# Kernel optimization log

Measured on AMD Instinct MI355X. Metric: run time of the kernel, lower is better.

## Reference

```python
import jax, jax.numpy as jnp
import numpy as np

N = 50000        # nodes
E = 1_600_000    # edges
F_IN = 128
HID = 128
OUT = 128
NEG_SLOPE = 0.2  # PyG GATConv default


def _gat_layer(x, src, dst, W, a_src, a_dst, b, n_nodes):
    """PyG GATConv (heads=1, add_self_loops handled by caller)."""
    h = x @ W                                   # [N, d_out]
    alpha_src = h @ a_src                       # [N]
    alpha_dst = h @ a_dst                       # [N]
    e = jax.nn.leaky_relu(alpha_src[src] + alpha_dst[dst], NEG_SLOPE)  # [E']
    # segment softmax over incoming edges of each destination node
    m = jax.ops.segment_max(e, dst, num_segments=n_nodes)
    e = jnp.exp(e - m[dst])
    s = jax.ops.segment_sum(e, dst, num_segments=n_nodes)
    alpha = e / s[dst]                          # [E']
    out = jax.ops.segment_sum(alpha[:, None] * h[src], dst, num_segments=n_nodes)
    return out + b


def setup_inputs() -> dict:
    key = jax.random.key(0)
    ks = jax.random.split(key, 11)
    sW1 = 1.0 / np.sqrt(F_IN)
    sW2 = 1.0 / np.sqrt(HID)
    return {
        "x": jax.random.normal(ks[0], (N, F_IN), dtype=jnp.float32),
        "edge_index": jax.random.randint(ks[1], (2, E), 0, N, dtype=jnp.int64
                                         if jax.config.jax_enable_x64 else jnp.int32),
        "W1": jax.random.normal(ks[2], (F_IN, HID), dtype=jnp.float32) * sW1,
        "a1_src": jax.random.normal(ks[3], (HID,), dtype=jnp.float32) * sW2,
        "a1_dst": jax.random.normal(ks[4], (HID,), dtype=jnp.float32) * sW2,
        "b1": jnp.zeros((HID,), dtype=jnp.float32),
        "W2": jax.random.normal(ks[5], (HID, OUT), dtype=jnp.float32) * sW2,
        "a2_src": jax.random.normal(ks[6], (OUT,), dtype=jnp.float32) * sW2,
        "a2_dst": jax.random.normal(ks[7], (OUT,), dtype=jnp.float32) * sW2,
        "b2": jnp.zeros((OUT,), dtype=jnp.float32),
    }


def reference(x, edge_index, W1, a1_src, a1_dst, b1, W2, a2_src, a2_dst, b2):
    n = x.shape[0]
    loop = jnp.arange(n, dtype=edge_index.dtype)
    src = jnp.concatenate([edge_index[0], loop])   # add self loops (PyG default)
    dst = jnp.concatenate([edge_index[1], loop])
    h = _gat_layer(x, src, dst, W1, a1_src, a1_dst, b1, n)
    h = jax.nn.relu(h)
    # F.dropout with training=False is identity (eval-mode reference)
    out = _gat_layer(h, src, dst, W2, a2_src, a2_dst, b2, n)
    return out
```

## Files before the change

### kernel.cpp

```cpp
#include <hip/hip_runtime.h>
#include <hip/hip_bf16.h>
#include <hip/hip_fp16.h>

#define FD 128
#define CBW 64
#define NB_MAX 1024

typedef _Float16 half8 __attribute__((ext_vector_type(8)));
typedef float f32x4 __attribute__((ext_vector_type(4)));

__global__ __launch_bounds__(256) void k_chist(const int* __restrict__ dst,
                                               int* __restrict__ ccnt, int e, int nb) {
    __shared__ int lh[NB_MAX];
    for (int i = threadIdx.x; i < nb; i += 256) lh[i] = 0;
    __syncthreads();
    for (int i = blockIdx.x * 256 + threadIdx.x; i < e; i += gridDim.x * 256)
        atomicAdd(&lh[dst[i] >> 6], 1);
    __syncthreads();
    for (int i = threadIdx.x; i < nb; i += 256) {
        int c = lh[i];
        if (c) atomicAdd(&ccnt[i], c);
    }
}

__global__ void k_cscan(const int* __restrict__ ccnt, int* __restrict__ cbase,
                        int* __restrict__ ccur, int nb, int* __restrict__ rowptr, int n) {
    __shared__ int wsum[16];
    __shared__ int woff[17];
    const int t = threadIdx.x, lane = t & 63, wid = t >> 6;
    int carry = 0;
    for (int base = 0; base < nb; base += 1024) {
        int idx = base + t;
        int v = (idx < nb) ? ccnt[idx] : 0;
        int s = v;
#pragma unroll
        for (int off = 1; off < 64; off <<= 1) {
            int u = __shfl_up(s, off, 64);
            if (lane >= off) s += u;
        }
        if (lane == 63) wsum[wid] = s;
        __syncthreads();
        if (wid == 0) {
            int w2 = (lane < 16) ? wsum[lane] : 0;
#pragma unroll
            for (int off = 1; off < 16; off <<= 1) {
                int u = __shfl_up(w2, off, 64);
                if (lane >= off) w2 += u;
            }
            if (lane < 16) woff[lane + 1] = w2;
            if (lane == 0) woff[0] = 0;
        }
        __syncthreads();
        int excl = carry + woff[wid] + (s - v);
        if (idx < nb) { cbase[idx] = excl; ccur[idx] = excl; }
        carry += woff[16];
        __syncthreads();
    }
    if (t == 0) { cbase[nb] = carry; rowptr[n] = carry; }
}

__global__ __launch_bounds__(256) void k_cscatter(const int* __restrict__ src,
                                                  const int* __restrict__ dst,
                                                  int* __restrict__ ccur,
                                                  int* __restrict__ ebuf,
                                                  int e, int nb, int nblocks) {
    __shared__ int lh[NB_MAX];
    __shared__ int lb[NB_MAX];
    const int per = (e + nblocks - 1) / nblocks;
    const int lo = blockIdx.x * per;
    const int hi = min(e, lo + per);
    const int t = threadIdx.x;
    for (int i = t; i < nb; i += 256) lh[i] = 0;
    __syncthreads();
    for (int i = lo + t; i < hi; i += 256) atomicAdd(&lh[dst[i] >> 6], 1);
    __syncthreads();
    for (int i = t; i < nb; i += 256) {
        int c = lh[i];
        lb[i] = c ? atomicAdd(&ccur[i], c) : 0;
    }
    __syncthreads();
    for (int i = t; i < nb; i += 256) lh[i] = 0;
    __syncthreads();
    for (int i = lo + t; i < hi; i += 256) {
        int d = dst[i];
        int bkt = d >> 6;
        int r = atomicAdd(&lh[bkt], 1);
        ebuf[lb[bkt] + r] = (src[i] << 6) | (d & (CBW - 1));
    }
}

__global__ __launch_bounds__(256) void k_fine(const int* __restrict__ ebuf,
                                              const int* __restrict__ cbase,
                                              int* __restrict__ rowptr,
                                              int* __restrict__ colidx, int n) {
    const int b = blockIdx.x;
    const int node0 = b * CBW;
    const int nloc = min(CBW, n - node0);
    const int beg = cbase[b], end = cbase[b + 1];
    __shared__ int fh[CBW];
    __shared__ int fo[CBW];
    const int t = threadIdx.x;
    if (t < CBW) fh[t] = 0;
    __syncthreads();
    for (int e = beg + t; e < end; e += 256) atomicAdd(&fh[ebuf[e] & (CBW - 1)], 1);
    __syncthreads();
    if (t < 64) {
        int v = fh[t];
        int s = v;
#pragma unroll
        for (int off = 1; off < 64; off <<= 1) {
            int u = __shfl_up(s, off, 64);
            if (t >= off) s += u;
        }
        fo[t] = s - v;
    }
    __syncthreads();
    if (t < nloc) rowptr[node0 + t] = beg + fo[t];
    if (t < CBW) fh[t] = 0;
    __syncthreads();
    for (int e = beg + t; e < end; e += 256) {
        int v = ebuf[e];
        int d = v & (CBW - 1);
        int r = atomicAdd(&fh[d], 1);
        colidx[beg + fo[d] + r] = v >> 6;
    }
}

__global__ __launch_bounds__(1024) void k_prep(const float* __restrict__ W1,
                                               const float* __restrict__ W2,
                                               __half* __restrict__ T1,
                                               __half* __restrict__ T2,
                                               const float* __restrict__ x,
                                               __half* __restrict__ x16, int count8) {
    const int t = threadIdx.x;
    if (blockIdx.x < 2) {
        __shared__ float sw[128 * 129];
        const float* W = blockIdx.x ? W2 : W1;
        __half* T = blockIdx.x ? T2 : T1;
#pragma unroll
        for (int i = 0; i < 16; i++) {
            int idx = i * 1024 + t;
            sw[(idx >> 7) * 129 + (idx & 127)] = W[idx];
        }
        __syncthreads();
#pragma unroll
        for (int i = 0; i < 8; i++) {
            int o = i * 1024 + t;
            int c = o >> 6, kp = o & 63;
            float lo = sw[(kp * 2) * 129 + c];
            float hi = sw[(kp * 2 + 1) * 129 + c];
            *(__half2*)&T[c * 128 + kp * 2] = __floats2half2_rn(lo, hi);
        }
    } else {
        int i = (blockIdx.x - 2) * 1024 + t;
        if (i >= count8) return;
        float4 a = *(const float4*)&x[(size_t)i * 8];
        float4 b = *(const float4*)&x[(size_t)i * 8 + 4];
        union { __half2 h2[4]; uint4 u; } pk;
        pk.h2[0] = __floats2half2_rn(a.x, a.y);
        pk.h2[1] = __floats2half2_rn(a.z, a.w);
        pk.h2[2] = __floats2half2_rn(b.x, b.y);
        pk.h2[3] = __floats2half2_rn(b.z, b.w);
        *(uint4*)&x16[(size_t)i * 8] = pk.u;
    }
}

__global__ __launch_bounds__(256) void k_gemm(const __half* __restrict__ X,
                                              const __half* __restrict__ Wt,
                                              const float* __restrict__ a_s,
                                              const float* __restrict__ a_d,
                                              __half* __restrict__ H,
                                              float* __restrict__ as_,
                                              float* __restrict__ ad_, int n) {
    const int t = threadIdx.x;
    const int wave = t >> 6, lane = t & 63;
    const int g = lane >> 4, c16 = lane & 15;
    const int row0 = blockIdx.x * 64 + wave * 16;

    half8 A[4];
    {
        int row = row0 + c16;
        int rc = (row < n) ? row : (n - 1);
        const __half* xp = &X[(size_t)rc * 128 + g * 8];
#pragma unroll
        for (int kc = 0; kc < 4; kc++) A[kc] = *(const half8*)(xp + kc * 32);
    }

    f32x4 acc[8];
#pragma unroll
    for (int ct = 0; ct < 8; ct++) acc[ct] = (f32x4){0.f, 0.f, 0.f, 0.f};

#pragma unroll
    for (int ct = 0; ct < 8; ct++) {
        const __half* wp = &Wt[(ct * 16 + c16) * 128 + g * 8];
#pragma unroll
        for (int kc = 0; kc < 4; kc++) {
            half8 b = *(const half8*)(wp + kc * 32);
            acc[ct] = __builtin_amdgcn_mfma_f32_16x16x32_f16(A[kc], b, acc[ct], 0, 0, 0);
        }
    }

    float asv[8], adv[8];
#pragma unroll
    for (int ct = 0; ct < 8; ct++) {
        asv[ct] = a_s[ct * 16 + c16];
        adv[ct] = a_d[ct * 16 + c16];
    }
#pragma unroll
    for (int r = 0; r < 4; r++) {
        const int row = row0 + g * 4 + r;
        float vs = 0.f, vd = 0.f;
#pragma unroll
        for (int ct = 0; ct < 8; ct++) {
            float v = acc[ct][r];
            vs += v * asv[ct];
            vd += v * adv[ct];
            if (row < n) H[(size_t)row * 128 + ct * 16 + c16] = __float2half(v);
        }
#pragma unroll
        for (int off = 8; off; off >>= 1) {
            vs += __shfl_xor(vs, off, 16);
            vd += __shfl_xor(vd, off, 16);
        }
        if (c16 == 0 && row < n) { as_[row] = vs; ad_[row] = vd; }
    }
}

__device__ __forceinline__ void fmix8(float* acc, uint4 hv, float w) {
    union { uint4 u; _Float16 h[8]; } c;
    c.u = hv;
#pragma unroll
    for (int j = 0; j < 8; j++) acc[j] += w * (float)c.h[j];
}

__global__ __launch_bounds__(256) void k_aggr(const __half* __restrict__ H,
                                              const float* __restrict__ as_,
                                              const float* __restrict__ ad_,
                                              const int* __restrict__ rowptr,
                                              const int* __restrict__ colidx,
                                              const float* __restrict__ bias,
                                              float* __restrict__ outf,
                                              __half* __restrict__ outh,
                                              int n, int mode) {
    const int wid = threadIdx.x >> 6;
    const int lane = threadIdx.x & 63;
    const int node = blockIdx.x * 4 + wid;
    if (node >= n) return;
    const int q = lane >> 4;
    const int boff = (lane & 15) * 16;
    const float adn = ad_[node];
    float sp = 0.f;
    float acc[8] = {0.f, 0.f, 0.f, 0.f, 0.f, 0.f, 0.f, 0.f};
    const int beg = rowptr[node], end = rowptr[node + 1];

    {
        float e = as_[node] + adn;
        e = (e > 0.f) ? e : 0.2f * e;
        const float w = __expf(e);
        if (lane == 63) sp += w;
        if (q == 3) {
            const uint4 hv = *(const uint4*)((const char*)H + (((unsigned)node << 8) + boff));
            fmix8(acc, hv, w);
        }
    }

    for (int it = beg; it < end; it += 64) {
        const int idx = it + lane;
        const bool valid = idx < end;
        const int idxc = valid ? idx : (end - 1);
        const int sl = colidx[idxc];
        float e = as_[sl] + adn;
        e = (e > 0.f) ? e : 0.2f * e;
        const float w = valid ? __expf(e) : 0.f;
        sp += w;
        int m = end - it; if (m > 64) m = 64;
        const int iters = (m + 3) >> 2;
        int slot = q;
#pragma unroll 4
        for (int g = 0; g < iters; ++g) {
            const int srcg = __shfl(sl, slot, 64);
            const float wg = __shfl(w, slot, 64);
            const uint4 hv = *(const uint4*)((const char*)H + (((unsigned)srcg << 8) + boff));
            fmix8(acc, hv, wg);
            slot += 4;
        }
    }

#pragma unroll
    for (int off = 1; off < 64; off <<= 1) sp += __shfl_xor(sp, off);
#pragma unroll
    for (int off = 16; off <= 32; off <<= 1) {
#pragma unroll
        for (int j = 0; j < 8; j++) acc[j] += __shfl_xor(acc[j], off);
    }
    if (q == 0) {
        const int f0 = boff >> 1;
        const float inv = 1.f / sp;
        float o[8];
        const float4 b0 = *(const float4*)&bias[f0];
        const float4 b1 = *(const float4*)&bias[f0 + 4];
        o[0] = acc[0] * inv + b0.x; o[1] = acc[1] * inv + b0.y;
        o[2] = acc[2] * inv + b0.z; o[3] = acc[3] * inv + b0.w;
        o[4] = acc[4] * inv + b1.x; o[5] = acc[5] * inv + b1.y;
        o[6] = acc[6] * inv + b1.z; o[7] = acc[7] * inv + b1.w;
        if (mode == 1) {
#pragma unroll
            for (int j = 0; j < 8; j++) o[j] = fmaxf(o[j], 0.f);
            union { __half2 h2[4]; uint4 u; } pk;
            pk.h2[0] = __floats2half2_rn(o[0], o[1]);
            pk.h2[1] = __floats2half2_rn(o[2], o[3]);
            pk.h2[2] = __floats2half2_rn(o[4], o[5]);
            pk.h2[3] = __floats2half2_rn(o[6], o[7]);
            *(uint4*)&outh[(size_t)node * 128 + f0] = pk.u;
        } else {
            *(float4*)&outf[(size_t)node * 128 + f0] = make_float4(o[0], o[1], o[2], o[3]);
            *(float4*)&outf[(size_t)node * 128 + f0 + 4] = make_float4(o[4], o[5], o[6], o[7]);
        }
    }
}

extern "C" void kernel_launch(void* const* d_in, const int* in_sizes, int n_in,
                              void* d_out, int out_size, void* d_ws, size_t ws_size,
                              hipStream_t stream) {
    const float* x   = (const float*)d_in[0];
    const int*   ei  = (const int*)d_in[1];
    const float* W1  = (const float*)d_in[2];
    const float* a1s = (const float*)d_in[3];
    const float* a1d = (const float*)d_in[4];
    const float* b1  = (const float*)d_in[5];
    const float* W2  = (const float*)d_in[6];
    const float* a2s = (const float*)d_in[7];
    const float* a2d = (const float*)d_in[8];
    const float* b2  = (const float*)d_in[9];
    float* dout = (float*)d_out;

    const int n = in_sizes[0] / FD;
    const int E = in_sizes[1] / 2;
    const int* src = ei;
    const int* dst = ei + E;
    const int NB = (n + CBW - 1) / CBW;

    char* base = (char*)d_ws;
    __half* buf0  = (__half*)base;
    int*    ebuf  = (int*)base;
    __half* H     = (__half*)(base + (size_t)n * FD * sizeof(__half));
    float* as_    = (float*)((char*)H + (size_t)n * FD * sizeof(__half));
    float* ad_    = as_ + n;
    int*   rowptr = (int*)(ad_ + n);
    int*   ccnt   = rowptr + (n + 1);
    int*   cbase  = ccnt + NB;
    int*   ccur   = cbase + NB + 1;
    int*   colidx = ccur + NB;
    size_t wt_off = (((size_t)((char*)(colidx + E) - base)) + 15) & ~(size_t)15;
    __half* Wt1h  = (__half*)(base + wt_off);
    __half* Wt2h  = Wt1h + 128 * 128;

    hipMemsetAsync(ccnt, 0, (size_t)NB * sizeof(int), stream);
    k_chist<<<256, 256, 0, stream>>>(dst, ccnt, E, NB);
    k_cscan<<<1, 1024, 0, stream>>>(ccnt, cbase, ccur, NB, rowptr, n);
    const int SCAT_BLOCKS = 256;
    k_cscatter<<<SCAT_BLOCKS, 256, 0, stream>>>(src, dst, ccur, ebuf, E, NB, SCAT_BLOCKS);
    k_fine<<<NB, 256, 0, stream>>>(ebuf, cbase, rowptr, colidx, n);

    const int count8 = n * FD / 8;
    const int prep_grid = 2 + (count8 + 1023) / 1024;
    k_prep<<<prep_grid, 1024, 0, stream>>>(W1, W2, Wt1h, Wt2h, x, buf0, count8);

    const int gemm_grid = (n + 63) / 64;
    const int node_grid = (n + 3) / 4;

    k_gemm<<<gemm_grid, 256, 0, stream>>>(buf0, Wt1h, a1s, a1d, H, as_, ad_, n);
    k_aggr<<<node_grid, 256, 0, stream>>>(H, as_, ad_, rowptr, colidx, b1,
                                          nullptr, buf0, n, 1);

    k_gemm<<<gemm_grid, 256, 0, stream>>>(buf0, Wt2h, a2s, a2d, H, as_, ad_, n);
    k_aggr<<<node_grid, 256, 0, stream>>>(H, as_, ad_, rowptr, colidx, b2,
                                          dout, nullptr, n, 0);
}
```

Before: 237.9 us.

## Fuse CSR build stages with weight transpose and layer-1 GEMM, pack aggregation shuffles

Merges the destination histogram with the weight transpose/convert, and the edge scatter with the first-layer GEMM, in shared grids. The GEMM now reads fp32 x directly, so the separate x-to-fp16 conversion pass goes away. Bucket width grows from 64 to 256 nodes, which turns the coarse scan into a single pass and makes the fine sort work across full 256-thread blocks. In aggregation, the source index and the fp16-rounded edge weight are packed into one int, so only one shuffle is needed per gathered edge. The packing assumes node ids fit in 16 bits and adds fp16 rounding of the unnormalized attention weights, with a possible overflow risk.

```diff
diff --git a/kernel.cpp b/kernel.cpp
--- a/kernel.cpp
+++ b/kernel.cpp
@@ -3,23 +3,48 @@
 #include <hip/hip_fp16.h>
 
 #define FD 128
-#define CBW 64
-#define NB_MAX 1024
+#define CBW 256
+#define NBK 256
 
 typedef _Float16 half8 __attribute__((ext_vector_type(8)));
 typedef float f32x4 __attribute__((ext_vector_type(4)));
 
-__global__ __launch_bounds__(256) void k_chist(const int* __restrict__ dst,
-                                               int* __restrict__ ccnt, int e, int nb) {
-    __shared__ int lh[NB_MAX];
-    for (int i = threadIdx.x; i < nb; i += 256) lh[i] = 0;
-    __syncthreads();
-    for (int i = blockIdx.x * 256 + threadIdx.x; i < e; i += gridDim.x * 256)
-        atomicAdd(&lh[dst[i] >> 6], 1);
-    __syncthreads();
-    for (int i = threadIdx.x; i < nb; i += 256) {
-        int c = lh[i];
-        if (c) atomicAdd(&ccnt[i], c);
+__global__ __launch_bounds__(256) void k_pre(const int* __restrict__ dst,
+                                             int* __restrict__ ccnt, int e, int nb,
+                                             const float* __restrict__ W1,
+                                             const float* __restrict__ W2,
+                                             __half* __restrict__ T1,
+                                             __half* __restrict__ T2) {
+    __shared__ float sw[128 * 129];
+    const int t = threadIdx.x;
+    if (blockIdx.x < 256) {
+        int* lh = (int*)sw;
+        if (t < NBK) lh[t] = 0;
+        __syncthreads();
+        for (int i = blockIdx.x * 256 + t; i < e; i += 256 * 256)
+            atomicAdd(&lh[dst[i] >> 8], 1);
+        __syncthreads();
+        if (t < nb) {
+            int c = lh[t];
+            if (c) atomicAdd(&ccnt[t], c);
+        }
+    } else {
+        const float* W = (blockIdx.x == 257) ? W2 : W1;
+        __half* T = (blockIdx.x == 257) ? T2 : T1;
+#pragma unroll
+        for (int i = 0; i < 64; i++) {
+            int idx = i * 256 + t;
+            sw[(idx >> 7) * 129 + (idx & 127)] = W[idx];
+        }
+        __syncthreads();
+#pragma unroll
+        for (int i = 0; i < 32; i++) {
+            int o = i * 256 + t;
+            int c = o >> 6, kp = o & 63;
+            float lo = sw[(kp * 2) * 129 + c];
+            float hi = sw[(kp * 2 + 1) * 129 + c];
+            *(__half2*)&T[c * 128 + kp * 2] = __floats2half2_rn(lo, hi);
+        }
     }
 }
 
@@ -28,64 +53,126 @@
     __shared__ int wsum[16];
     __shared__ int woff[17];
     const int t = threadIdx.x, lane = t & 63, wid = t >> 6;
-    int carry = 0;
-    for (int base = 0; base < nb; base += 1024) {
-        int idx = base + t;
-        int v = (idx < nb) ? ccnt[idx] : 0;
-        int s = v;
-#pragma unroll
-        for (int off = 1; off < 64; off <<= 1) {
-            int u = __shfl_up(s, off, 64);
-            if (lane >= off) s += u;
-        }
-        if (lane == 63) wsum[wid] = s;
-        __syncthreads();
-        if (wid == 0) {
-            int w2 = (lane < 16) ? wsum[lane] : 0;
-#pragma unroll
-            for (int off = 1; off < 16; off <<= 1) {
-                int u = __shfl_up(w2, off, 64);
-                if (lane >= off) w2 += u;
+    int v = (t < nb) ? ccnt[t] : 0;
+    int s = v;
+#pragma unroll
+    for (int off = 1; off < 64; off <<= 1) {
+        int u = __shfl_up(s, off, 64);
+        if (lane >= off) s += u;
+    }
+    if (lane == 63) wsum[wid] = s;
+    __syncthreads();
+    if (wid == 0) {
+        int w2 = (lane < 16) ? wsum[lane] : 0;
+#pragma unroll
+        for (int off = 1; off < 16; off <<= 1) {
+            int u = __shfl_up(w2, off, 64);
+            if (lane >= off) w2 += u;
+        }
+        if (lane < 16) woff[lane + 1] = w2;
+        if (lane == 0) woff[0] = 0;
+    }
+    __syncthreads();
+    int excl = woff[wid] + (s - v);
+    if (t < nb) { cbase[t] = excl; ccur[t] = excl; }
+    if (t == 0) { cbase[nb] = woff[16]; rowptr[n] = woff[16]; }
+}
+
+__global__ __launch_bounds__(256) void k_mid(const int* __restrict__ src,
+                                             const int* __restrict__ dst,
+                                             int* __restrict__ ccur,
+                                             int* __restrict__ ebuf,
+                                             int e, int nb, int nscat,
+                                             const float* __restrict__ X,
+                                             const __half* __restrict__ Wt,
+                                             const float* __restrict__ a_s,
+                                             const float* __restrict__ a_d,
+                                             __half* __restrict__ H,
+                                             float* __restrict__ as_,
+                                             float* __restrict__ ad_, int n) {
+    __shared__ int lh[NBK];
+    __shared__ int lb[NBK];
+    const int t = threadIdx.x;
+    if ((int)blockIdx.x < nscat) {
+        const int per = (e + nscat - 1) / nscat;
+        const int lo = blockIdx.x * per;
+        const int hi = min(e, lo + per);
+        if (t < NBK) lh[t] = 0;
+        __syncthreads();
+        for (int i = lo + t; i < hi; i += 256) atomicAdd(&lh[dst[i] >> 8], 1);
+        __syncthreads();
+        if (t < nb) {
+            int c = lh[t];
+            lb[t] = c ? atomicAdd(&ccur[t], c) : 0;
+        }
+        __syncthreads();
+        if (t < NBK) lh[t] = 0;
+        __syncthreads();
+        for (int i = lo + t; i < hi; i += 256) {
+            int d = dst[i];
+            int bkt = d >> 8;
+            int r = atomicAdd(&lh[bkt], 1);
+            ebuf[lb[bkt] + r] = (src[i] << 8) | (d & (CBW - 1));
+        }
+    } else {
+        const int bid = blockIdx.x - nscat;
+        const int wave = t >> 6, lane = t & 63;
+        const int g = lane >> 4, c16 = lane & 15;
+        const int row0 = bid * 64 + wave * 16;
+
+        half8 A[4];
+        {
+            int row = row0 + c16;
+            int rc = (row < n) ? row : (n - 1);
+            const float* xp = &X[(size_t)rc * 128 + g * 8];
+#pragma unroll
+            for (int kc = 0; kc < 4; kc++) {
+                float4 x0 = *(const float4*)(xp + kc * 32);
+                float4 x1 = *(const float4*)(xp + kc * 32 + 4);
+                half8 a;
+                a[0] = (_Float16)x0.x; a[1] = (_Float16)x0.y;
+                a[2] = (_Float16)x0.z; a[3] = (_Float16)x0.w;
+                a[4] = (_Float16)x1.x; a[5] = (_Float16)x1.y;
+                a[6] = (_Float16)x1.z; a[7] = (_Float16)x1.w;
+                A[kc] = a;
             }
-            if (lane < 16) woff[lane + 1] = w2;
-            if (lane == 0) woff[0] = 0;
-        }
-        __syncthreads();
-        int excl = carry + woff[wid] + (s - v);
-        if (idx < nb) { cbase[idx] = excl; ccur[idx] = excl; }
-        carry += woff[16];
-        __syncthreads();
-    }
-    if (t == 0) { cbase[nb] = carry; rowptr[n] = carry; }
-}
-
-__global__ __launch_bounds__(256) void k_cscatter(const int* __restrict__ src,
-                                                  const int* __restrict__ dst,
-                                                  int* __restrict__ ccur,
-                                                  int* __restrict__ ebuf,
-                                                  int e, int nb, int nblocks) {
-    __shared__ int lh[NB_MAX];
-    __shared__ int lb[NB_MAX];
-    const int per = (e + nblocks - 1) / nblocks;
-    const int lo = blockIdx.x * per;
-    const int hi = min(e, lo + per);
-    const int t = threadIdx.x;
-    for (int i = t; i < nb; i += 256) lh[i] = 0;
-    __syncthreads();
-    for (int i = lo + t; i < hi; i += 256) atomicAdd(&lh[dst[i] >> 6], 1);
-    __syncthreads();
-    for (int i = t; i < nb; i += 256) {
-        int c = lh[i];
-        lb[i] = c ? atomicAdd(&ccur[i], c) : 0;
-    }
-    __syncthreads();
-    for (int i = t; i < nb; i += 256) lh[i] = 0;
-    __syncthreads();
-    for (int i = lo + t; i < hi; i += 256) {
-        int d = dst[i];
-        int bkt = d >> 6;
-        int r = atomicAdd(&lh[bkt], 1);
-        ebuf[lb[bkt] + r] = (src[i] << 6) | (d & (CBW - 1));
+        }
+        f32x4 acc[8];
+#pragma unroll
+        for (int ct = 0; ct < 8; ct++) acc[ct] = (f32x4){0.f, 0.f, 0.f, 0.f};
+#pragma unroll
+        for (int ct = 0; ct < 8; ct++) {
+            const __half* wp = &Wt[(ct * 16 + c16) * 128 + g * 8];
+#pragma unroll
+            for (int kc = 0; kc < 4; kc++) {
+                half8 b = *(const half8*)(wp + kc * 32);
+                acc[ct] = __builtin_amdgcn_mfma_f32_16x16x32_f16(A[kc], b, acc[ct], 0, 0, 0);
+            }
+        }
+        float asv[8], adv[8];
+#pragma unroll
+        for (int ct = 0; ct < 8; ct++) {
+            asv[ct] = a_s[ct * 16 + c16];
+            adv[ct] = a_d[ct * 16 + c16];
+        }
+#pragma unroll
+        for (int r = 0; r < 4; r++) {
+            const int row = row0 + g * 4 + r;
+            float vs = 0.f, vd = 0.f;
+#pragma unroll
+            for (int ct = 0; ct < 8; ct++) {
+                float v = acc[ct][r];
+                vs += v * asv[ct];
+                vd += v * adv[ct];
+                if (row < n) H[(size_t)row * 128 + ct * 16 + c16] = __float2half(v);
+            }
+#pragma unroll
+            for (int off = 8; off; off >>= 1) {
+                vs += __shfl_xor(vs, off, 16);
+                vd += __shfl_xor(vd, off, 16);
+            }
+            if (c16 == 0 && row < n) { as_[row] = vs; ad_[row] = vd; }
+        }
     }
 }
 
@@ -99,69 +186,36 @@
     const int beg = cbase[b], end = cbase[b + 1];
     __shared__ int fh[CBW];
     __shared__ int fo[CBW];
-    const int t = threadIdx.x;
-    if (t < CBW) fh[t] = 0;
+    __shared__ int wt4[4];
+    const int t = threadIdx.x, lane = t & 63, wid = t >> 6;
+    fh[t] = 0;
     __syncthreads();
     for (int e = beg + t; e < end; e += 256) atomicAdd(&fh[ebuf[e] & (CBW - 1)], 1);
     __syncthreads();
-    if (t < 64) {
+    {
         int v = fh[t];
         int s = v;
 #pragma unroll
         for (int off = 1; off < 64; off <<= 1) {
             int u = __shfl_up(s, off, 64);
-            if (t >= off) s += u;
-        }
-        fo[t] = s - v;
+            if (lane >= off) s += u;
+        }
+        if (lane == 63) wt4[wid] = s;
+        __syncthreads();
+        int wo = 0;
+#pragma unroll
+        for (int j = 0; j < 4; j++) wo += (j < wid) ? wt4[j] : 0;
+        fo[t] = wo + s - v;
     }
     __syncthreads();
     if (t < nloc) rowptr[node0 + t] = beg + fo[t];
-    if (t < CBW) fh[t] = 0;
+    fh[t] = 0;
     __syncthreads();
     for (int e = beg + t; e < end; e += 256) {
         int v = ebuf[e];
         int d = v & (CBW - 1);
         int r = atomicAdd(&fh[d], 1);
-        colidx[beg + fo[d] + r] = v >> 6;
-    }
-}
-
-__global__ __launch_bounds__(1024) void k_prep(const float* __restrict__ W1,
-                                               const float* __restrict__ W2,
-                                               __half* __restrict__ T1,
-                                               __half* __restrict__ T2,
-                                               const float* __restrict__ x,
-                                               __half* __restrict__ x16, int count8) {
-    const int t = threadIdx.x;
-    if (blockIdx.x < 2) {
-        __shared__ float sw[128 * 129];
-        const float* W = blockIdx.x ? W2 : W1;
-        __half* T = blockIdx.x ? T2 : T1;
-#pragma unroll
-        for (int i = 0; i < 16; i++) {
-            int idx = i * 1024 + t;
-            sw[(idx >> 7) * 129 + (idx & 127)] = W[idx];
-        }
-        __syncthreads();
-#pragma unroll
-        for (int i = 0; i < 8; i++) {
-            int o = i * 1024 + t;
-            int c = o >> 6, kp = o & 63;
-            float lo = sw[(kp * 2) * 129 + c];
-            float hi = sw[(kp * 2 + 1) * 129 + c];
-            *(__half2*)&T[c * 128 + kp * 2] = __floats2half2_rn(lo, hi);
-        }
-    } else {
-        int i = (blockIdx.x - 2) * 1024 + t;
-        if (i >= count8) return;
-        float4 a = *(const float4*)&x[(size_t)i * 8];
-        float4 b = *(const float4*)&x[(size_t)i * 8 + 4];
-        union { __half2 h2[4]; uint4 u; } pk;
-        pk.h2[0] = __floats2half2_rn(a.x, a.y);
-        pk.h2[1] = __floats2half2_rn(a.z, a.w);
-        pk.h2[2] = __floats2half2_rn(b.x, b.y);
-        pk.h2[3] = __floats2half2_rn(b.z, b.w);
-        *(uint4*)&x16[(size_t)i * 8] = pk.u;
+        colidx[beg + fo[d] + r] = v >> 8;
     }
 }
 
@@ -185,11 +239,9 @@
 #pragma unroll
         for (int kc = 0; kc < 4; kc++) A[kc] = *(const half8*)(xp + kc * 32);
     }
-
     f32x4 acc[8];
 #pragma unroll
     for (int ct = 0; ct < 8; ct++) acc[ct] = (f32x4){0.f, 0.f, 0.f, 0.f};
-
 #pragma unroll
     for (int ct = 0; ct < 8; ct++) {
         const __half* wp = &Wt[(ct * 16 + c16) * 128 + g * 8];
@@ -199,7 +251,6 @@
             acc[ct] = __builtin_amdgcn_mfma_f32_16x16x32_f16(A[kc], b, acc[ct], 0, 0, 0);
         }
     }
-
     float asv[8], adv[8];
 #pragma unroll
     for (int ct = 0; ct < 8; ct++) {
@@ -273,14 +324,16 @@
         e = (e > 0.f) ? e : 0.2f * e;
         const float w = valid ? __expf(e) : 0.f;
         sp += w;
+        const int pk = (sl << 16) | (int)__half_as_ushort(__float2half(w));
         int m = end - it; if (m > 64) m = 64;
         const int iters = (m + 3) >> 2;
         int slot = q;
 #pragma unroll 4
         for (int g = 0; g < iters; ++g) {
-            const int srcg = __shfl(sl, slot, 64);
-            const float wg = __shfl(w, slot, 64);
-            const uint4 hv = *(const uint4*)((const char*)H + (((unsigned)srcg << 8) + boff));
+            const int pg = __shfl(pk, slot, 64);
+            const unsigned srcg = ((unsigned)pg) >> 16;
+            const float wg = __half2float(__ushort_as_half((unsigned short)(pg & 0xffff)));
+            const uint4 hv = *(const uint4*)((const char*)H + ((srcg << 8) + boff));
             fmix8(acc, hv, wg);
             slot += 4;
         }
@@ -306,12 +359,12 @@
         if (mode == 1) {
 #pragma unroll
             for (int j = 0; j < 8; j++) o[j] = fmaxf(o[j], 0.f);
-            union { __half2 h2[4]; uint4 u; } pk;
-            pk.h2[0] = __floats2half2_rn(o[0], o[1]);
-            pk.h2[1] = __floats2half2_rn(o[2], o[3]);
-            pk.h2[2] = __floats2half2_rn(o[4], o[5]);
-            pk.h2[3] = __floats2half2_rn(o[6], o[7]);
-            *(uint4*)&outh[(size_t)node * 128 + f0] = pk.u;
+            union { __half2 h2[4]; uint4 u; } pkk;
+            pkk.h2[0] = __floats2half2_rn(o[0], o[1]);
+            pkk.h2[1] = __floats2half2_rn(o[2], o[3]);
+            pkk.h2[2] = __floats2half2_rn(o[4], o[5]);
+            pkk.h2[3] = __floats2half2_rn(o[6], o[7]);
+            *(uint4*)&outh[(size_t)node * 128 + f0] = pkk.u;
         } else {
             *(float4*)&outf[(size_t)node * 128 + f0] = make_float4(o[0], o[1], o[2], o[3]);
             *(float4*)&outf[(size_t)node * 128 + f0 + 4] = make_float4(o[4], o[5], o[6], o[7]);
@@ -355,24 +408,18 @@
     __half* Wt1h  = (__half*)(base + wt_off);
     __half* Wt2h  = Wt1h + 128 * 128;
 
-    hipMemsetAsync(ccnt, 0, (size_t)NB * sizeof(int), stream);
-    k_chist<<<256, 256, 0, stream>>>(dst, ccnt, E, NB);
-    k_cscan<<<1, 1024, 0, stream>>>(ccnt, cbase, ccur, NB, rowptr, n);
-    const int SCAT_BLOCKS = 256;
-    k_cscatter<<<SCAT_BLOCKS, 256, 0, stream>>>(src, dst, ccur, ebuf, E, NB, SCAT_BLOCKS);
-    k_fine<<<NB, 256, 0, stream>>>(ebuf, cbase, rowptr, colidx, n);
-
-    const int count8 = n * FD / 8;
-    const int prep_grid = 2 + (count8 + 1023) / 1024;
-    k_prep<<<prep_grid, 1024, 0, stream>>>(W1, W2, Wt1h, Wt2h, x, buf0, count8);
-
     const int gemm_grid = (n + 63) / 64;
     const int node_grid = (n + 3) / 4;
-
-    k_gemm<<<gemm_grid, 256, 0, stream>>>(buf0, Wt1h, a1s, a1d, H, as_, ad_, n);
+    const int SCAT = 256;
+
+    hipMemsetAsync(ccnt, 0, (size_t)NB * sizeof(int), stream);
+    k_pre<<<258, 256, 0, stream>>>(dst, ccnt, E, NB, W1, W2, Wt1h, Wt2h);
+    k_cscan<<<1, 1024, 0, stream>>>(ccnt, cbase, ccur, NB, rowptr, n);
+    k_mid<<<SCAT + gemm_grid, 256, 0, stream>>>(src, dst, ccur, ebuf, E, NB, SCAT,
+                                                x, Wt1h, a1s, a1d, H, as_, ad_, n);
+    k_fine<<<NB, 256, 0, stream>>>(ebuf, cbase, rowptr, colidx, n);
     k_aggr<<<node_grid, 256, 0, stream>>>(H, as_, ad_, rowptr, colidx, b1,
                                           nullptr, buf0, n, 1);
-
     k_gemm<<<gemm_grid, 256, 0, stream>>>(buf0, Wt2h, a2s, a2d, H, as_, ad_, n);
     k_aggr<<<node_grid, 256, 0, stream>>>(H, as_, ad_, rowptr, colidx, b2,
                                           dout, nullptr, n, 0);
```

Measured after the change: 226.8 us. 1.05x faster.
